# Kernel optimization log

Measured on AMD Instinct MI355X. Metric: run time of the kernel, lower is better.

Reference implementation:

```python
import jax, jax.numpy as jnp
import numpy as np

N_PARTICLES = 128
D = 2048


def setup_inputs() -> dict:
    key = jax.random.key(0)
    k1, k2 = jax.random.split(key)
    var_flat = jax.random.normal(k1, (N_PARTICLES, D), dtype=jnp.float32)
    grad_flat = jax.random.normal(k2, (N_PARTICLES, D), dtype=jnp.float32)
    return {"var_flat": var_flat, "grad_flat": grad_flat}


def reference(var_flat, grad_flat):
    # SVGD gradient correction for one particle variable, as in SteinModel.train_step.
    n, d = var_flat.shape
    # M = grad^T grad / n  -> [d, d] metric
    M = jnp.matmul(grad_flat.T, grad_flat) / n
    # sign_diff[i, j, :] = var_flat[j] - var_flat[i]  (TF broadcasting of x - x[:, None])
    sign_diff = var_flat[None, :, :] - var_flat[:, None, :]  # [n, n, d]
    Msd = jnp.einsum('ijd,de->ije', sign_diff, M)  # [n, n, d]
    dMsd = jnp.sum(sign_diff * Msd, axis=2)  # [n, n]
    # median bandwidth: tfp.stats.percentile default interpolation is 'nearest'
    med = jnp.percentile(dMsd, 50.0, method='nearest')
    h = med ** 2 / np.float32(np.log(n))
    kern = jnp.exp(-dMsd / (2.0 * h))  # [n, n]
    # gkern = -einsum('ijd,ij->idj', Msd, kern) / h ; mgJ = kern @ grad - sum_j gkern
    mgJ = jnp.matmul(kern, grad_flat) + jnp.einsum('ijd,ij->id', Msd, kern) / h
    return mgJ
```

## Files before the change

kernel.cpp:

```cpp
#include <hip/hip_runtime.h>
#include <math.h>

#define NP 128
#define DIM 2048

__global__ __launch_bounds__(256) void k_pmat(const float* __restrict__ var,
                                              const float* __restrict__ grad,
                                              float* __restrict__ P) {
    __shared__ float At[32][132];
    __shared__ float Bt[32][132];
    const int tid = threadIdx.x;
    const int k0  = blockIdx.x * 32;

    for (int c = tid; c < 1024; c += 256) {
        const int row = c >> 3;
        const int kq  = (c & 7) << 2;
        const float4 a = *(const float4*)(var  + row * DIM + k0 + kq);
        const float4 b = *(const float4*)(grad + row * DIM + k0 + kq);
        At[kq + 0][row] = a.x; At[kq + 1][row] = a.y;
        At[kq + 2][row] = a.z; At[kq + 3][row] = a.w;
        Bt[kq + 0][row] = b.x; Bt[kq + 1][row] = b.y;
        Bt[kq + 2][row] = b.z; Bt[kq + 3][row] = b.w;
    }
    __syncthreads();

    const int tx = tid & 15;
    const int ty = tid >> 4;
    float acc[8][8] = {};

    #pragma unroll 4
    for (int kk = 0; kk < 32; ++kk) {
        float a[8], b[8];
        #pragma unroll
        for (int i = 0; i < 8; ++i) a[i] = At[kk][ty + 16 * i];
        #pragma unroll
        for (int j = 0; j < 8; ++j) b[j] = Bt[kk][tx + 16 * j];
        #pragma unroll
        for (int i = 0; i < 8; ++i)
            #pragma unroll
            for (int j = 0; j < 8; ++j)
                acc[i][j] = fmaf(a[i], b[j], acc[i][j]);
    }

    #pragma unroll
    for (int i = 0; i < 8; ++i)
        #pragma unroll
        for (int j = 0; j < 8; ++j)
            unsafeAtomicAdd(&P[(ty + 16 * i) * NP + (tx + 16 * j)], acc[i][j]);
}

__global__ __launch_bounds__(128) void k_dmsd(const float* __restrict__ P,
                                              float* __restrict__ dMsd) {
    __shared__ float Pi[NP];
    const int i = blockIdx.x;
    const int j = threadIdx.x;
    Pi[j] = P[i * NP + j];
    __syncthreads();
    float acc = 0.f;
    #pragma unroll 4
    for (int k = 0; k < NP; k += 4) {
        const float4 p = *(const float4*)&P[j * NP + k];
        const float d0 = p.x - Pi[k + 0];
        const float d1 = p.y - Pi[k + 1];
        const float d2 = p.z - Pi[k + 2];
        const float d3 = p.w - Pi[k + 3];
        acc = fmaf(d0, d0, acc);
        acc = fmaf(d1, d1, acc);
        acc = fmaf(d2, d2, acc);
        acc = fmaf(d3, d3, acc);
    }
    dMsd[i * NP + j] = acc * (1.0f / 128.0f);
}

__global__ __launch_bounds__(1024) void k_median(const float* __restrict__ dMsd,
                                                 float* __restrict__ scal) {
    __shared__ unsigned warp_sums[16];
    __shared__ unsigned sh_lo;
    const int tid = threadIdx.x;
    unsigned v[16];
    #pragma unroll
    for (int u = 0; u < 16; ++u)
        v[u] = __float_as_uint(dMsd[tid + u * 1024]);
    if (tid == 0) sh_lo = 0u;
    __syncthreads();

    unsigned lo = 0u;
    for (int b = 30; b >= 0; --b) {
        const unsigned mid = lo | (1u << b);
        unsigned cnt = 0;
        #pragma unroll
        for (int u = 0; u < 16; ++u) cnt += (v[u] < mid) ? 1u : 0u;
        #pragma unroll
        for (int o = 32; o > 0; o >>= 1) cnt += __shfl_down(cnt, o);
        if ((tid & 63) == 0) warp_sums[tid >> 6] = cnt;
        __syncthreads();
        if (tid == 0) {
            unsigned total = 0;
            #pragma unroll
            for (int w = 0; w < 16; ++w) total += warp_sums[w];
            if (total <= 8192u) sh_lo = mid;
        }
        __syncthreads();
        lo = sh_lo;
    }

    if (tid == 0) {
        const float med = __uint_as_float(lo);
        const float h = med * med * (1.0f / 4.852030263919617f);
        scal[0] = med;
        scal[1] = 1.0f / (2.0f * h);
        scal[2] = 1.0f / h;
    }
}

__global__ __launch_bounds__(128) void k_amat(const float* __restrict__ P,
                                              const float* __restrict__ dMsd,
                                              const float* __restrict__ scal,
                                              float* __restrict__ A) {
    __shared__ float kern[NP];
    __shared__ float wsum[2];
    const int i = blockIdx.x;
    const int j = threadIdx.x;
    const float inv2h = scal[1];
    const float invh  = scal[2];
    const float kv = expf(-dMsd[i * NP + j] * inv2h);
    kern[j] = kv;
    float s = kv;
    #pragma unroll
    for (int o = 32; o > 0; o >>= 1) s += __shfl_down(s, o);
    if ((j & 63) == 0) wsum[j >> 6] = s;
    __syncthreads();
    const float rowsum = wsum[0] + wsum[1];
    float acc = 0.f;
    for (int m = 0; m < NP; ++m)
        acc = fmaf(kern[m], P[m * NP + j], acc);
    A[i * NP + j] = kern[j] + invh * (1.0f / 128.0f) * (acc - rowsum * P[i * NP + j]);
}

__global__ __launch_bounds__(256) void k_out(const float* __restrict__ A,
                                             const float* __restrict__ grad,
                                             float* __restrict__ out) {
    __shared__ float Al[8][128];
    const int tid   = threadIdx.x;
    const int c     = (blockIdx.x << 6) + (tid & 63);
    const int rbase = blockIdx.y << 3;
    const int q     = tid >> 6;
    for (int idx = tid; idx < 1024; idx += 256)
        Al[idx >> 7][idx & 127] = A[(rbase + (idx >> 7)) * NP + (idx & 127)];
    __syncthreads();
    const int r0 = q * 2, r1 = q * 2 + 1;
    float acc0 = 0.f, acc1 = 0.f;
    for (int m = 0; m < NP; ++m) {
        const float g = grad[m * DIM + c];
        acc0 = fmaf(Al[r0][m], g, acc0);
        acc1 = fmaf(Al[r1][m], g, acc1);
    }
    out[(rbase + r0) * DIM + c] = acc0;
    out[(rbase + r1) * DIM + c] = acc1;
}

extern "C" void kernel_launch(void* const* d_in, const int* in_sizes, int n_in,
                              void* d_out, int out_size, void* d_ws, size_t ws_size,
                              hipStream_t stream) {
    const float* var  = (const float*)d_in[0];
    const float* grad = (const float*)d_in[1];
    float* out  = (float*)d_out;

    float* P    = (float*)d_ws;
    float* dMsd = P + NP * NP;
    float* A    = dMsd + NP * NP;
    float* scal = A + NP * NP;

    hipMemsetAsync(P, 0, NP * NP * sizeof(float), stream);
    k_pmat  <<<dim3(64),     dim3(256),  0, stream>>>(var, grad, P);
    k_dmsd  <<<dim3(NP),     dim3(NP),   0, stream>>>(P, dMsd);
    k_median<<<dim3(1),      dim3(1024), 0, stream>>>(dMsd, scal);
    k_amat  <<<dim3(NP),     dim3(NP),   0, stream>>>(P, dMsd, scal, A);
    k_out   <<<dim3(32, 16), dim3(256),  0, stream>>>(A, grad, out);
}
```

Before: 104.0 us.

## Fuse all stages into one cooperative kernel with grid-wide syncs

Replaces the memset and five separate launches with a single cooperative kernel of 64 blocks that separates the stages with grid.sync(). Each block writes its partial P product to its own slice of workspace instead of using atomics, and a separate pass then sums the slices. The dMsd stage now keeps its value in a register and reuses the full P matrix held in shared memory for the A-matrix stage. The goal is to remove launch overhead and atomic contention, at the cost of grid-barrier latency, 64 partial-product buffers of extra workspace traffic, and a median stage that runs on one block while the others wait.

```diff
diff --git a/kernel.cpp b/kernel.cpp
--- a/kernel.cpp
+++ b/kernel.cpp
@@ -1,162 +1,179 @@
 #include <hip/hip_runtime.h>
+#include <hip/hip_cooperative_groups.h>
 #include <math.h>
 
-#define NP 128
-#define DIM 2048
+namespace cg = cooperative_groups;
 
-__global__ __launch_bounds__(256) void k_pmat(const float* __restrict__ var,
-                                              const float* __restrict__ grad,
-                                              float* __restrict__ P) {
-    __shared__ float At[32][132];
-    __shared__ float Bt[32][132];
+#define NP   128
+#define DIM  2048
+#define NBLK 64
+#define NTHR 256
+
+__global__ __launch_bounds__(NTHR) void stein_fused(
+    const float* __restrict__ var, const float* __restrict__ grad,
+    float* __restrict__ out, float* __restrict__ Ppart,
+    float* __restrict__ P, float* __restrict__ dMsd,
+    float* __restrict__ A, float* __restrict__ scal)
+{
+    cg::grid_group grid = cg::this_grid();
+
+    __shared__ float smem[16512];
+    __shared__ float kern_s[2 * NP];
+    __shared__ float wsum[4];
+    __shared__ unsigned usmall[8];
+
     const int tid = threadIdx.x;
-    const int k0  = blockIdx.x * 32;
+    const int b   = blockIdx.x;
 
-    for (int c = tid; c < 1024; c += 256) {
-        const int row = c >> 3;
-        const int kq  = (c & 7) << 2;
-        const float4 a = *(const float4*)(var  + row * DIM + k0 + kq);
-        const float4 b = *(const float4*)(grad + row * DIM + k0 + kq);
-        At[kq + 0][row] = a.x; At[kq + 1][row] = a.y;
-        At[kq + 2][row] = a.z; At[kq + 3][row] = a.w;
-        Bt[kq + 0][row] = b.x; Bt[kq + 1][row] = b.y;
-        Bt[kq + 2][row] = b.z; Bt[kq + 3][row] = b.w;
-    }
-    __syncthreads();
+    {
+        float* At = smem;
+        float* Bt = smem + 32 * 132;
+        const int k0 = b * 32;
+        for (int c = tid; c < 1024; c += NTHR) {
+            const int row = c >> 3;
+            const int kq  = (c & 7) << 2;
+            const float4 a = *(const float4*)(var  + row * DIM + k0 + kq);
+            const float4 g = *(const float4*)(grad + row * DIM + k0 + kq);
+            At[(kq + 0) * 132 + row] = a.x; At[(kq + 1) * 132 + row] = a.y;
+            At[(kq + 2) * 132 + row] = a.z; At[(kq + 3) * 132 + row] = a.w;
+            Bt[(kq + 0) * 132 + row] = g.x; Bt[(kq + 1) * 132 + row] = g.y;
+            Bt[(kq + 2) * 132 + row] = g.z; Bt[(kq + 3) * 132 + row] = g.w;
+        }
+        __syncthreads();
 
-    const int tx = tid & 15;
-    const int ty = tid >> 4;
-    float acc[8][8] = {};
-
-    #pragma unroll 4
-    for (int kk = 0; kk < 32; ++kk) {
-        float a[8], b[8];
-        #pragma unroll
-        for (int i = 0; i < 8; ++i) a[i] = At[kk][ty + 16 * i];
-        #pragma unroll
-        for (int j = 0; j < 8; ++j) b[j] = Bt[kk][tx + 16 * j];
+        const int tx = tid & 15;
+        const int ty = tid >> 4;
+        float acc[8][8] = {};
+        #pragma unroll 4
+        for (int kk = 0; kk < 32; ++kk) {
+            float a[8], g[8];
+            #pragma unroll
+            for (int i = 0; i < 8; ++i) a[i] = At[kk * 132 + ty + 16 * i];
+            #pragma unroll
+            for (int j = 0; j < 8; ++j) g[j] = Bt[kk * 132 + tx + 16 * j];
+            #pragma unroll
+            for (int i = 0; i < 8; ++i)
+                #pragma unroll
+                for (int j = 0; j < 8; ++j)
+                    acc[i][j] = fmaf(a[i], g[j], acc[i][j]);
+        }
+        float* dst = Ppart + b * (NP * NP);
         #pragma unroll
         for (int i = 0; i < 8; ++i)
             #pragma unroll
             for (int j = 0; j < 8; ++j)
-                acc[i][j] = fmaf(a[i], b[j], acc[i][j]);
+                dst[(ty + 16 * i) * NP + tx + 16 * j] = acc[i][j];
     }
+    grid.sync();
 
-    #pragma unroll
-    for (int i = 0; i < 8; ++i)
-        #pragma unroll
-        for (int j = 0; j < 8; ++j)
-            unsafeAtomicAdd(&P[(ty + 16 * i) * NP + (tx + 16 * j)], acc[i][j]);
-}
+    {
+        const int tg = b * NTHR + tid;
+        float s = 0.f;
+        #pragma unroll 8
+        for (int p = 0; p < NBLK; ++p) s += Ppart[p * (NP * NP) + tg];
+        P[tg] = s;
+    }
+    grid.sync();
 
-__global__ __launch_bounds__(128) void k_dmsd(const float* __restrict__ P,
-                                              float* __restrict__ dMsd) {
-    __shared__ float Pi[NP];
-    const int i = blockIdx.x;
-    const int j = threadIdx.x;
-    Pi[j] = P[i * NP + j];
-    __syncthreads();
-    float acc = 0.f;
-    #pragma unroll 4
-    for (int k = 0; k < NP; k += 4) {
-        const float4 p = *(const float4*)&P[j * NP + k];
-        const float d0 = p.x - Pi[k + 0];
-        const float d1 = p.y - Pi[k + 1];
-        const float d2 = p.z - Pi[k + 2];
-        const float d3 = p.w - Pi[k + 3];
-        acc = fmaf(d0, d0, acc);
-        acc = fmaf(d1, d1, acc);
-        acc = fmaf(d2, d2, acc);
-        acc = fmaf(d3, d3, acc);
-    }
-    dMsd[i * NP + j] = acc * (1.0f / 128.0f);
-}
-
-__global__ __launch_bounds__(1024) void k_median(const float* __restrict__ dMsd,
-                                                 float* __restrict__ scal) {
-    __shared__ unsigned warp_sums[16];
-    __shared__ unsigned sh_lo;
-    const int tid = threadIdx.x;
-    unsigned v[16];
-    #pragma unroll
-    for (int u = 0; u < 16; ++u)
-        v[u] = __float_as_uint(dMsd[tid + u * 1024]);
-    if (tid == 0) sh_lo = 0u;
-    __syncthreads();
-
-    unsigned lo = 0u;
-    for (int b = 30; b >= 0; --b) {
-        const unsigned mid = lo | (1u << b);
-        unsigned cnt = 0;
-        #pragma unroll
-        for (int u = 0; u < 16; ++u) cnt += (v[u] < mid) ? 1u : 0u;
-        #pragma unroll
-        for (int o = 32; o > 0; o >>= 1) cnt += __shfl_down(cnt, o);
-        if ((tid & 63) == 0) warp_sums[tid >> 6] = cnt;
-        __syncthreads();
-        if (tid == 0) {
-            unsigned total = 0;
-            #pragma unroll
-            for (int w = 0; w < 16; ++w) total += warp_sums[w];
-            if (total <= 8192u) sh_lo = mid;
+    float my_dmsd;
+    {
+        for (int f = tid; f < 4096; f += NTHR) {
+            const float4 v4 = *(const float4*)(P + 4 * f);
+            const int r = f >> 5;
+            const int c = (4 * f) & 127;
+            smem[r * 129 + c + 0] = v4.x; smem[r * 129 + c + 1] = v4.y;
+            smem[r * 129 + c + 2] = v4.z; smem[r * 129 + c + 3] = v4.w;
         }
         __syncthreads();
-        lo = sh_lo;
+        const int i = 2 * b + (tid >> 7);
+        const int j = tid & 127;
+        float acc = 0.f;
+        #pragma unroll 4
+        for (int k = 0; k < NP; ++k) {
+            const float d = smem[i * 129 + k] - smem[j * 129 + k];
+            acc = fmaf(d, d, acc);
+        }
+        my_dmsd = acc * (1.0f / 128.0f);
+        dMsd[b * NTHR + tid] = my_dmsd;
     }
+    grid.sync();
 
-    if (tid == 0) {
-        const float med = __uint_as_float(lo);
-        const float h = med * med * (1.0f / 4.852030263919617f);
-        scal[0] = med;
-        scal[1] = 1.0f / (2.0f * h);
-        scal[2] = 1.0f / h;
+    if (b == 0) {
+        unsigned v[64];
+        #pragma unroll
+        for (int u = 0; u < 64; ++u) v[u] = __float_as_uint(dMsd[u * NTHR + tid]);
+        if (tid == 0) usmall[4] = 0u;
+        __syncthreads();
+        unsigned lo = 0u;
+        for (int bit = 30; bit >= 0; --bit) {
+            const unsigned mid = lo | (1u << bit);
+            unsigned cnt = 0;
+            #pragma unroll
+            for (int u = 0; u < 64; ++u) cnt += (v[u] < mid) ? 1u : 0u;
+            #pragma unroll
+            for (int o = 32; o > 0; o >>= 1) cnt += __shfl_down(cnt, o);
+            if ((tid & 63) == 0) usmall[tid >> 6] = cnt;
+            __syncthreads();
+            if (tid == 0) {
+                const unsigned total = usmall[0] + usmall[1] + usmall[2] + usmall[3];
+                if (total <= 8192u) usmall[4] = mid;
+            }
+            __syncthreads();
+            lo = usmall[4];
+        }
+        if (tid == 0) {
+            const float med = __uint_as_float(lo);
+            const float h = med * med * (1.0f / 4.852030263919617f);
+            scal[0] = med;
+            scal[1] = 1.0f / (2.0f * h);
+            scal[2] = 1.0f / h;
+        }
     }
-}
+    grid.sync();
 
-__global__ __launch_bounds__(128) void k_amat(const float* __restrict__ P,
-                                              const float* __restrict__ dMsd,
-                                              const float* __restrict__ scal,
-                                              float* __restrict__ A) {
-    __shared__ float kern[NP];
-    __shared__ float wsum[2];
-    const int i = blockIdx.x;
-    const int j = threadIdx.x;
-    const float inv2h = scal[1];
-    const float invh  = scal[2];
-    const float kv = expf(-dMsd[i * NP + j] * inv2h);
-    kern[j] = kv;
-    float s = kv;
-    #pragma unroll
-    for (int o = 32; o > 0; o >>= 1) s += __shfl_down(s, o);
-    if ((j & 63) == 0) wsum[j >> 6] = s;
-    __syncthreads();
-    const float rowsum = wsum[0] + wsum[1];
-    float acc = 0.f;
-    for (int m = 0; m < NP; ++m)
-        acc = fmaf(kern[m], P[m * NP + j], acc);
-    A[i * NP + j] = kern[j] + invh * (1.0f / 128.0f) * (acc - rowsum * P[i * NP + j]);
-}
+    {
+        const float inv2h = scal[1];
+        const float invh  = scal[2];
+        const int h = tid >> 7;
+        const int i = 2 * b + h;
+        const int j = tid & 127;
+        const float kv = expf(-my_dmsd * inv2h);
+        kern_s[h * NP + j] = kv;
+        float s = kv;
+        #pragma unroll
+        for (int o = 32; o > 0; o >>= 1) s += __shfl_down(s, o);
+        if ((tid & 63) == 0) wsum[tid >> 6] = s;
+        __syncthreads();
+        const float rowsum = wsum[2 * h] + wsum[2 * h + 1];
+        float acc = 0.f;
+        #pragma unroll 4
+        for (int m = 0; m < NP; ++m)
+            acc = fmaf(kern_s[h * NP + m], smem[m * 129 + j], acc);
+        A[i * NP + j] = kv + invh * (1.0f / 128.0f) * (acc - rowsum * smem[i * 129 + j]);
+    }
+    grid.sync();
 
-__global__ __launch_bounds__(256) void k_out(const float* __restrict__ A,
-                                             const float* __restrict__ grad,
-                                             float* __restrict__ out) {
-    __shared__ float Al[8][128];
-    const int tid   = threadIdx.x;
-    const int c     = (blockIdx.x << 6) + (tid & 63);
-    const int rbase = blockIdx.y << 3;
-    const int q     = tid >> 6;
-    for (int idx = tid; idx < 1024; idx += 256)
-        Al[idx >> 7][idx & 127] = A[(rbase + (idx >> 7)) * NP + (idx & 127)];
-    __syncthreads();
-    const int r0 = q * 2, r1 = q * 2 + 1;
-    float acc0 = 0.f, acc1 = 0.f;
-    for (int m = 0; m < NP; ++m) {
-        const float g = grad[m * DIM + c];
-        acc0 = fmaf(Al[r0][m], g, acc0);
-        acc1 = fmaf(Al[r1][m], g, acc1);
+    {
+        const int rg = b >> 3;
+        const int cgp = b & 7;
+        for (int f = tid; f < 512; f += NTHR) {
+            const float4 a4 = *(const float4*)(A + rg * 16 * NP + 4 * f);
+            smem[4 * f + 0] = a4.x; smem[4 * f + 1] = a4.y;
+            smem[4 * f + 2] = a4.z; smem[4 * f + 3] = a4.w;
+        }
+        __syncthreads();
+        const int c = cgp * 256 + tid;
+        float acc[16] = {};
+        for (int m = 0; m < NP; ++m) {
+            const float g = grad[m * DIM + c];
+            #pragma unroll
+            for (int r = 0; r < 16; ++r)
+                acc[r] = fmaf(smem[r * NP + m], g, acc[r]);
+        }
+        #pragma unroll
+        for (int r = 0; r < 16; ++r)
+            out[(rg * 16 + r) * DIM + c] = acc[r];
     }
-    out[(rbase + r0) * DIM + c] = acc0;
-    out[(rbase + r1) * DIM + c] = acc1;
 }
 
 extern "C" void kernel_launch(void* const* d_in, const int* in_sizes, int n_in,
@@ -164,17 +181,17 @@
                               hipStream_t stream) {
     const float* var  = (const float*)d_in[0];
     const float* grad = (const float*)d_in[1];
-    float* out  = (float*)d_out;
+    float* out = (float*)d_out;
 
-    float* P    = (float*)d_ws;
-    float* dMsd = P + NP * NP;
-    float* A    = dMsd + NP * NP;
-    float* scal = A + NP * NP;
+    float* Ppart = (float*)d_ws;
+    float* P     = Ppart + NBLK * NP * NP;
+    float* dMsd  = P + NP * NP;
+    float* A     = dMsd + NP * NP;
+    float* scal  = A + NP * NP;
 
-    hipMemsetAsync(P, 0, NP * NP * sizeof(float), stream);
-    k_pmat  <<<dim3(64),     dim3(256),  0, stream>>>(var, grad, P);
-    k_dmsd  <<<dim3(NP),     dim3(NP),   0, stream>>>(P, dMsd);
-    k_median<<<dim3(1),      dim3(1024), 0, stream>>>(dMsd, scal);
-    k_amat  <<<dim3(NP),     dim3(NP),   0, stream>>>(P, dMsd, scal, A);
-    k_out   <<<dim3(32, 16), dim3(256),  0, stream>>>(A, grad, out);
+    void* args[] = { (void*)&var, (void*)&grad, (void*)&out,
+                     (void*)&Ppart, (void*)&P, (void*)&dMsd,
+                     (void*)&A, (void*)&scal };
+    hipLaunchCooperativeKernel((const void*)stein_fused, dim3(NBLK), dim3(NTHR),
+                               args, 0, stream);
 }
```

Result: slower. 169.0 us (+62.5%).
